# Kernel tuning notes

Hardware: AMD Instinct MI355X
Metric: run time of the kernel (lower is better)

The kernel has to match this reference:

```python
import jax, jax.numpy as jnp
import numpy as np

B, T, D, H = 8, 4096, 1024, 8  # batch, seq_len, width, num_heads


def setup_inputs() -> dict:
    key = jax.random.key(0)
    k0, k1, k2, k3 = jax.random.split(key, 4)
    bw = D // H
    std = (1.0 / bw) ** 0.5  # w_init_variance_scale=1.0
    x = jax.random.normal(k0, (B, T, D), dtype=jnp.float32)
    segment_pos = jnp.tile(jnp.arange(T, dtype=jnp.int32)[None, :], (B, 1))
    ig_w = (jax.random.normal(k1, (H, bw, bw), dtype=jnp.float32) * std)
    ig_b = jnp.zeros((H, bw), dtype=jnp.float32)
    ag_w = (jax.random.normal(k2, (H, bw, bw), dtype=jnp.float32) * std)
    ag_b = jnp.zeros((H, bw), dtype=jnp.float32)
    # rnn_param_init: a_param = log(u^{-0.5} - 1), u ~ U(min_rad^2+eps, max_rad^2+eps)
    eps = 1e-8
    u = jax.random.uniform(k3, (D,), minval=0.9 ** 2 + eps, maxval=0.999 ** 2 + eps)
    a_param = jnp.log(jnp.exp(-0.5 * jnp.log(u)) - 1.0).astype(jnp.float32)
    return dict(x=x, segment_pos=segment_pos, a_param=a_param,
                ig_w=ig_w, ig_b=ig_b, ag_w=ag_w, ag_b=ag_b)


def _block_linear(x, w, b):
    # x: [B,T,D] -> blocks [B,T,H,bw]; y = x_blocks @ w[h] + b[h]
    Bx, Tx, Dx = x.shape
    h, bw = w.shape[0], w.shape[1]
    xb = x.reshape(Bx, Tx, h, bw)
    y = jnp.einsum('bthi,hij->bthj', xb, w) + b
    return y.reshape(Bx, Tx, Dx)


def _rglru(x, a_param, ig_w, ig_b, ag_w, ag_b, sqrt_fn):
    gate_x = jax.nn.sigmoid(_block_linear(x, ig_w, ig_b))
    gate_a = jax.nn.sigmoid(_block_linear(x, ag_w, ag_b))
    log_a = -8.0 * gate_a * jax.nn.softplus(a_param)  # [B,T,D]
    a = jnp.exp(log_a)
    a2 = jnp.exp(2.0 * log_a)
    multiplier = sqrt_fn(jnp.maximum(1.0 - a2, 1e-7))
    normed_x = x * gate_x * multiplier
    # closed-form scan: h_t = p_{t} * sum_{s<=t} normed_x_s / p_s, p = prefix cumprod of a
    p = jnp.cumprod(a, axis=1)
    p_prefix = jnp.concatenate([jnp.ones_like(p[:, :1]), p[:, :-1]], axis=1)
    p_prefix = jnp.maximum(p_prefix, 1e-7)
    S = jnp.cumsum(normed_x / p_prefix, axis=1)
    h = p_prefix * S  # h0 = 0 so alpha term vanishes
    return h, h[:, -1, :]


def reference(x, segment_pos, a_param, ig_w, ig_b, ag_w, ag_b):
    y, last_h = _rglru(x, a_param, ig_w, ig_b, ag_w, ag_b, jnp.sqrt)
    return y, last_h
```

## Files before the change

kernel.cpp:

```cpp
#include <hip/hip_runtime.h>
#include <math.h>

namespace {
constexpr int B = 8, T = 4096, D = 1024, H = 8, BW = 128;
constexpr int C = 128;
constexpr int L = T / C;
constexpr size_t BCD = (size_t)B * C * D;
constexpr size_t BTD = (size_t)B * T * D;
constexpr int WFRAG_N = H * 2 * 2 * 4 * 8 * 64 * 8;

typedef __attribute__((ext_vector_type(8))) short short8v;
typedef __attribute__((ext_vector_type(4))) float float4v;

__device__ __forceinline__ float fast_rcp(float x) { return __builtin_amdgcn_rcpf(x); }
__device__ __forceinline__ float fast_sigmoid(float z) {
    return fast_rcp(1.f + __expf(-z));
}
__device__ __forceinline__ unsigned short bf16_trunc(float x) {
    return (unsigned short)(__float_as_uint(x) >> 16);
}
__device__ __forceinline__ float bf16_tof(unsigned short u) {
    return __uint_as_float((unsigned)u << 16);
}
}

__global__ void k0_wsplit(const float* __restrict__ ig_w,
                          const float* __restrict__ ag_w,
                          unsigned short* __restrict__ wfrag)
{
    const int idx  = blockIdx.x * 256 + threadIdx.x;
    const int e    = idx & 7;
    const int lane = (idx >> 3) & 63;
    const int nt   = (idx >> 9) & 7;
    const int kt   = (idx >> 12) & 3;
    const int s    = (idx >> 14) & 1;
    const int g    = (idx >> 15) & 1;
    const int h    = (idx >> 16) & 7;
    const int k = kt * 32 + (lane >> 4) * 8 + e;
    const int n = nt * 16 + (lane & 15);
    const float w = (g ? ag_w : ig_w)[(size_t)h * BW * BW + (size_t)k * BW + n];
    const unsigned short hi = bf16_trunc(w);
    wfrag[idx] = s ? bf16_trunc(w - bf16_tof(hi)) : hi;
}

__global__ __launch_bounds__(256) void k1_gates(
    const float* __restrict__ x, const float* __restrict__ a_param,
    const float* __restrict__ ig_b, const float* __restrict__ ag_b,
    const unsigned short* __restrict__ wfrag,
    float* __restrict__ log_a, float* __restrict__ nx_out,
    float* __restrict__ logSum)
{
    __shared__ unsigned short xsh[L * BW];
    __shared__ unsigned short xsl[L * BW];

    const int bid = blockIdx.x;
    const int h   = bid & 7;
    const int c   = (bid >> 3) & (C - 1);
    const int b   = bid >> 10;
    const int tid  = threadIdx.x;
    const int wid  = tid >> 6;
    const int lane = tid & 63;
    const int t0   = c * L;

    for (int u = tid; u < L * 32; u += 256) {
        const int row = u >> 5;
        const int c4  = (u & 31) * 4;
        const float4 v = *(const float4*)&x[((size_t)(b * T + t0 + row)) * D + h * BW + c4];
        const float vv[4] = {v.x, v.y, v.z, v.w};
        short4 hv, lv;
        {
            unsigned short h0 = bf16_trunc(vv[0]), h1 = bf16_trunc(vv[1]);
            unsigned short h2 = bf16_trunc(vv[2]), h3 = bf16_trunc(vv[3]);
            hv.x = (short)h0; hv.y = (short)h1; hv.z = (short)h2; hv.w = (short)h3;
            lv.x = (short)bf16_trunc(vv[0] - bf16_tof(h0));
            lv.y = (short)bf16_trunc(vv[1] - bf16_tof(h1));
            lv.z = (short)bf16_trunc(vv[2] - bf16_tof(h2));
            lv.w = (short)bf16_trunc(vv[3] - bf16_tof(h3));
        }
        unsigned byte = (unsigned)(row * 256 + c4 * 2);
        byte ^= (unsigned)((row & 7) << 4);
        *(short4*)((char*)xsh + byte) = hv;
        *(short4*)((char*)xsl + byte) = lv;
    }
    __syncthreads();

    const float4v zero4 = {0.f, 0.f, 0.f, 0.f};
    float4v acc[2][2][2];
    #pragma unroll
    for (int g = 0; g < 2; ++g)
        #pragma unroll
        for (int mt = 0; mt < 2; ++mt)
            #pragma unroll
            for (int ntl = 0; ntl < 2; ++ntl) acc[g][mt][ntl] = zero4;

    #pragma unroll
    for (int kt = 0; kt < 4; ++kt) {
        short8v a[2][2];
        #pragma unroll
        for (int mt = 0; mt < 2; ++mt) {
            const int r = mt * 16 + (lane & 15);
            unsigned byte = (unsigned)(r * 256 + kt * 64 + (lane >> 4) * 16);
            byte ^= (unsigned)((r & 7) << 4);
            a[mt][0] = *(const short8v*)((const char*)xsh + byte);
            a[mt][1] = *(const short8v*)((const char*)xsl + byte);
        }
        short8v bb[2][2][2];
        #pragma unroll
        for (int g = 0; g < 2; ++g)
            #pragma unroll
            for (int ntl = 0; ntl < 2; ++ntl)
                #pragma unroll
                for (int s = 0; s < 2; ++s) {
                    const int ntg = wid * 2 + ntl;
                    const size_t fi =
                        ((((((size_t)h * 2 + g) * 2 + s) * 4 + kt) * 8 + ntg) * 64 + lane) * 8;
                    bb[g][ntl][s] = *(const short8v*)&wfrag[fi];
                }
        #pragma unroll
        for (int g = 0; g < 2; ++g)
            #pragma unroll
            for (int mt = 0; mt < 2; ++mt)
                #pragma unroll
                for (int ntl = 0; ntl < 2; ++ntl) {
                    acc[g][mt][ntl] = __builtin_amdgcn_mfma_f32_16x16x32_bf16(
                        a[mt][0], bb[g][ntl][0], acc[g][mt][ntl], 0, 0, 0);
                    acc[g][mt][ntl] = __builtin_amdgcn_mfma_f32_16x16x32_bf16(
                        a[mt][0], bb[g][ntl][1], acc[g][mt][ntl], 0, 0, 0);
                    acc[g][mt][ntl] = __builtin_amdgcn_mfma_f32_16x16x32_bf16(
                        a[mt][1], bb[g][ntl][0], acc[g][mt][ntl], 0, 0, 0);
                }
    }

    float sp2[2], bi2[2], ba2[2], csum[2] = {0.f, 0.f};
    #pragma unroll
    for (int ntl = 0; ntl < 2; ++ntl) {
        const int col = wid * 32 + ntl * 16 + (lane & 15);
        sp2[ntl] = log1pf(__expf(a_param[h * BW + col]));
        bi2[ntl] = ig_b[h * BW + col];
        ba2[ntl] = ag_b[h * BW + col];
    }
    #pragma unroll
    for (int mt = 0; mt < 2; ++mt)
        #pragma unroll
        for (int ntl = 0; ntl < 2; ++ntl) {
            const int col = wid * 32 + ntl * 16 + (lane & 15);
            #pragma unroll
            for (int e = 0; e < 4; ++e) {
                const int tl = mt * 16 + ((lane >> 4) & 3) * 4 + e;
                const float gx = fast_sigmoid(acc[0][mt][ntl][e] + bi2[ntl]);
                const float ga = fast_sigmoid(acc[1][mt][ntl][e] + ba2[ntl]);
                const float la = -8.f * ga * sp2[ntl];
                const float a2 = __expf(2.f * la);
                const float mu = sqrtf(fmaxf(1.f - a2, 1e-7f));
                unsigned byte = (unsigned)(tl * 256 + col * 2);
                byte ^= (unsigned)((tl & 7) << 4);
                const float xv =
                    bf16_tof(*(const unsigned short*)((const char*)xsh + byte)) +
                    bf16_tof(*(const unsigned short*)((const char*)xsl + byte));
                const size_t gi = ((size_t)(b * T + t0 + tl)) * D + h * BW + col;
                log_a[gi]  = la;
                nx_out[gi] = xv * gx * mu;
                csum[ntl] += la;
            }
        }
    #pragma unroll
    for (int ntl = 0; ntl < 2; ++ntl) {
        float v = csum[ntl];
        v += __shfl_xor(v, 16);
        v += __shfl_xor(v, 32);
        if ((lane & 48) == 0) {
            const int col = wid * 32 + ntl * 16 + lane;
            logSum[((size_t)(b * C + c)) * D + h * BW + col] = v;
        }
    }
}

__global__ void k_scan(float* __restrict__ s)
{
    const int g = blockIdx.x * blockDim.x + threadIdx.x;
    const int b = g >> 10, d = g & 1023;
    const size_t base = (size_t)b * C * D + d;
    float off = 0.f;
    for (int c0 = 0; c0 < C; c0 += 8) {
        float v[8];
        #pragma unroll
        for (int j = 0; j < 8; ++j) v[j] = s[base + (size_t)(c0 + j) * D];
        #pragma unroll
        for (int j = 0; j < 8; ++j) {
            s[base + (size_t)(c0 + j) * D] = off;
            off += v[j];
        }
    }
}

__global__ __launch_bounds__(256) void k3_zsum(
    const float* __restrict__ log_a, const float* __restrict__ nx,
    const float* __restrict__ logOff, float* __restrict__ Zsum)
{
    const int c = blockIdx.x & (C - 1), b = blockIdx.x >> 7;
    const int d = threadIdx.x * 4;
    const size_t cb = ((size_t)(b * C + c)) * D + d;
    float lp[4], zs[4] = {0.f, 0.f, 0.f, 0.f};
    *(float4*)lp = *(const float4*)&logOff[cb];
    size_t base = ((size_t)(b * T + c * L)) * D + d;
    float la4[4], nv4[4], lan[4], nvn[4];
    *(float4*)lan = *(const float4*)&log_a[base];
    *(float4*)nvn = *(const float4*)&nx[base];
    #pragma unroll 4
    for (int t = 0; t < L; ++t) {
        *(float4*)la4 = *(const float4*)lan;
        *(float4*)nv4 = *(const float4*)nvn;
        if (t + 1 < L) {
            *(float4*)lan = *(const float4*)&log_a[base + D];
            *(float4*)nvn = *(const float4*)&nx[base + D];
        }
        #pragma unroll
        for (int k = 0; k < 4; ++k) {
            const float qq = fmaxf(__expf(lp[k]), 1e-7f);
            zs[k] += nv4[k] * fast_rcp(qq);
            lp[k] += la4[k];
        }
        base += D;
    }
    *(float4*)&Zsum[cb] = *(const float4*)zs;
}

__global__ __launch_bounds__(256) void k5_final(
    const float* __restrict__ log_a, const float* __restrict__ logOff,
    const float* __restrict__ Zoff, float* y ,
    float* __restrict__ last_h)
{
    const int c = blockIdx.x & (C - 1), b = blockIdx.x >> 7;
    const int d = threadIdx.x * 4;
    const size_t cb = ((size_t)(b * C + c)) * D + d;
    float lp[4], S[4], h4[4] = {0.f, 0.f, 0.f, 0.f};
    *(float4*)lp = *(const float4*)&logOff[cb];
    *(float4*)S  = *(const float4*)&Zoff[cb];
    size_t base = ((size_t)(b * T + c * L)) * D + d;
    float la4[4], nv4[4], lan[4], nvn[4];
    *(float4*)lan = *(const float4*)&log_a[base];
    *(float4*)nvn = *(const float4*)&y[base];
    #pragma unroll 4
    for (int t = 0; t < L; ++t) {
        *(float4*)la4 = *(const float4*)lan;
        *(float4*)nv4 = *(const float4*)nvn;
        if (t + 1 < L) {
            *(float4*)lan = *(const float4*)&log_a[base + D];
            *(float4*)nvn = *(const float4*)&y[base + D];
        }
        #pragma unroll
        for (int k = 0; k < 4; ++k) {
            const float qq = fmaxf(__expf(lp[k]), 1e-7f);
            S[k] += nv4[k] * fast_rcp(qq);
            h4[k] = qq * S[k];
            lp[k] += la4[k];
        }
        *(float4*)&y[base] = *(const float4*)h4;
        base += D;
    }
    if (c == C - 1)
        *(float4*)&last_h[(size_t)b * D + d] = *(const float4*)h4;
}

extern "C" void kernel_launch(void* const* d_in, const int* in_sizes, int n_in,
                              void* d_out, int out_size, void* d_ws, size_t ws_size,
                              hipStream_t stream)
{
    const float* x       = (const float*)d_in[0];
    const float* a_param = (const float*)d_in[2];
    const float* ig_w    = (const float*)d_in[3];
    const float* ig_b    = (const float*)d_in[4];
    const float* ag_w    = (const float*)d_in[5];
    const float* ag_b    = (const float*)d_in[6];

    float* out    = (float*)d_out;
    float* y      = out;
    float* last_h = out + BTD;

    float* w    = (float*)d_ws;
    float* logS = w;
    float* Zs   = w + BCD;
    float* la   = w + 2 * BCD;
    unsigned short* wfrag = (unsigned short*)Zs;

    k0_wsplit<<<WFRAG_N / 256, 256, 0, stream>>>(ig_w, ag_w, wfrag);
    k1_gates <<<B * C * H, 256, 0, stream>>>(x, a_param, ig_b, ag_b, wfrag,
                                             la, y, logS);
    k_scan   <<<(B * D) / 256, 256, 0, stream>>>(logS);
    k3_zsum  <<<B * C, 256, 0, stream>>>(la, y, logS, Zs);
    k_scan   <<<(B * D) / 256, 256, 0, stream>>>(Zs);
    k5_final <<<B * C, 256, 0, stream>>>(la, logS, Zs, y, last_h);
}
```

Baseline: 431.8 us.

## Transpose chunk summaries, use wave-shuffle scan, and enlarge gate tiles with B prefetch

Stores the per-chunk log-sum and Z-sum arrays in a [B,D,C] layout. The chunk scan becomes a single-wave shuffle-based prefix over contiguous memory instead of a serial strided loop per column. The gate kernel now processes 64-row tiles with 512 threads (two halves of 32 rows) and prefetches the next k-step's weight fragments into registers. The scan kernels also use deeper unrolling. The cost is strided scalar loads and stores of the chunk summaries in k3/k5, plus higher register pressure in k1.

```diff
diff --git a/kernel.cpp b/kernel.cpp
--- a/kernel.cpp
+++ b/kernel.cpp
@@ -5,6 +5,7 @@
 constexpr int B = 8, T = 4096, D = 1024, H = 8, BW = 128;
 constexpr int C = 128;
 constexpr int L = T / C;
+constexpr int KROWS = 64;
 constexpr size_t BCD = (size_t)B * C * D;
 constexpr size_t BTD = (size_t)B * T * D;
 constexpr int WFRAG_N = H * 2 * 2 * 4 * 8 * 64 * 8;
@@ -43,26 +44,29 @@
     wfrag[idx] = s ? bf16_trunc(w - bf16_tof(hi)) : hi;
 }
 
-__global__ __launch_bounds__(256) void k1_gates(
+__global__ __launch_bounds__(512) void k1_gates(
     const float* __restrict__ x, const float* __restrict__ a_param,
     const float* __restrict__ ig_b, const float* __restrict__ ag_b,
     const unsigned short* __restrict__ wfrag,
     float* __restrict__ log_a, float* __restrict__ nx_out,
     float* __restrict__ logSum)
 {
-    __shared__ unsigned short xsh[L * BW];
-    __shared__ unsigned short xsl[L * BW];
-
-    const int bid = blockIdx.x;
-    const int h   = bid & 7;
-    const int c   = (bid >> 3) & (C - 1);
-    const int b   = bid >> 10;
-    const int tid  = threadIdx.x;
-    const int wid  = tid >> 6;
-    const int lane = tid & 63;
-    const int t0   = c * L;
-
-    for (int u = tid; u < L * 32; u += 256) {
+    __shared__ unsigned short xsh[KROWS * BW];
+    __shared__ unsigned short xsl[KROWS * BW];
+
+    const int bid  = blockIdx.x;
+    const int h    = bid & 7;
+    const int tile = (bid >> 3) & 63;
+    const int b    = bid >> 9;
+    const int tid   = threadIdx.x;
+    const int wid   = tid >> 6;
+    const int lane  = tid & 63;
+    const int half  = wid >> 2;
+    const int nquad = wid & 3;
+    const int t0    = tile * KROWS;
+    const int rbase = half * 32;
+
+    for (int u = tid; u < KROWS * 32; u += 512) {
         const int row = u >> 5;
         const int c4  = (u & 31) * 4;
         const float4 v = *(const float4*)&x[((size_t)(b * T + t0 + row)) * D + h * BW + c4];
@@ -93,29 +97,31 @@
             #pragma unroll
             for (int ntl = 0; ntl < 2; ++ntl) acc[g][mt][ntl] = zero4;
 
+#define LOADB(dst, ktv)                                                          \
+    _Pragma("unroll") for (int g = 0; g < 2; ++g)                                \
+    _Pragma("unroll") for (int ntl = 0; ntl < 2; ++ntl)                          \
+    _Pragma("unroll") for (int s = 0; s < 2; ++s) {                              \
+        const int ntg = nquad * 2 + ntl;                                         \
+        const size_t fi =                                                        \
+            ((((((size_t)h * 2 + g) * 2 + s) * 4 + (ktv)) * 8 + ntg) * 64 + lane) * 8; \
+        dst[g][ntl][s] = *(const short8v*)&wfrag[fi];                            \
+    }
+
+    short8v bb[2][2][2];
+    LOADB(bb, 0)
     #pragma unroll
     for (int kt = 0; kt < 4; ++kt) {
+        short8v bbn[2][2][2];
+        if (kt < 3) { LOADB(bbn, kt + 1) }
         short8v a[2][2];
         #pragma unroll
         for (int mt = 0; mt < 2; ++mt) {
-            const int r = mt * 16 + (lane & 15);
+            const int r = rbase + mt * 16 + (lane & 15);
             unsigned byte = (unsigned)(r * 256 + kt * 64 + (lane >> 4) * 16);
             byte ^= (unsigned)((r & 7) << 4);
             a[mt][0] = *(const short8v*)((const char*)xsh + byte);
             a[mt][1] = *(const short8v*)((const char*)xsl + byte);
         }
-        short8v bb[2][2][2];
-        #pragma unroll
-        for (int g = 0; g < 2; ++g)
-            #pragma unroll
-            for (int ntl = 0; ntl < 2; ++ntl)
-                #pragma unroll
-                for (int s = 0; s < 2; ++s) {
-                    const int ntg = wid * 2 + ntl;
-                    const size_t fi =
-                        ((((((size_t)h * 2 + g) * 2 + s) * 4 + kt) * 8 + ntg) * 64 + lane) * 8;
-                    bb[g][ntl][s] = *(const short8v*)&wfrag[fi];
-                }
         #pragma unroll
         for (int g = 0; g < 2; ++g)
             #pragma unroll
@@ -129,12 +135,21 @@
                     acc[g][mt][ntl] = __builtin_amdgcn_mfma_f32_16x16x32_bf16(
                         a[mt][1], bb[g][ntl][0], acc[g][mt][ntl], 0, 0, 0);
                 }
-    }
+        if (kt < 3) {
+            #pragma unroll
+            for (int g = 0; g < 2; ++g)
+                #pragma unroll
+                for (int ntl = 0; ntl < 2; ++ntl)
+                    #pragma unroll
+                    for (int s = 0; s < 2; ++s) bb[g][ntl][s] = bbn[g][ntl][s];
+        }
+    }
+#undef LOADB
 
     float sp2[2], bi2[2], ba2[2], csum[2] = {0.f, 0.f};
     #pragma unroll
     for (int ntl = 0; ntl < 2; ++ntl) {
-        const int col = wid * 32 + ntl * 16 + (lane & 15);
+        const int col = nquad * 32 + ntl * 16 + (lane & 15);
         sp2[ntl] = log1pf(__expf(a_param[h * BW + col]));
         bi2[ntl] = ig_b[h * BW + col];
         ba2[ntl] = ag_b[h * BW + col];
@@ -143,10 +158,10 @@
     for (int mt = 0; mt < 2; ++mt)
         #pragma unroll
         for (int ntl = 0; ntl < 2; ++ntl) {
-            const int col = wid * 32 + ntl * 16 + (lane & 15);
+            const int col = nquad * 32 + ntl * 16 + (lane & 15);
             #pragma unroll
             for (int e = 0; e < 4; ++e) {
-                const int tl = mt * 16 + ((lane >> 4) & 3) * 4 + e;
+                const int tl = rbase + mt * 16 + ((lane >> 4) & 3) * 4 + e;
                 const float gx = fast_sigmoid(acc[0][mt][ntl][e] + bi2[ntl]);
                 const float ga = fast_sigmoid(acc[1][mt][ntl][e] + ba2[ntl]);
                 const float la = -8.f * ga * sp2[ntl];
@@ -163,34 +178,37 @@
                 csum[ntl] += la;
             }
         }
+    const int cc = tile * 2 + half;
     #pragma unroll
     for (int ntl = 0; ntl < 2; ++ntl) {
         float v = csum[ntl];
         v += __shfl_xor(v, 16);
         v += __shfl_xor(v, 32);
         if ((lane & 48) == 0) {
-            const int col = wid * 32 + ntl * 16 + lane;
-            logSum[((size_t)(b * C + c)) * D + h * BW + col] = v;
-        }
-    }
-}
-
-__global__ void k_scan(float* __restrict__ s)
-{
-    const int g = blockIdx.x * blockDim.x + threadIdx.x;
-    const int b = g >> 10, d = g & 1023;
-    const size_t base = (size_t)b * C * D + d;
-    float off = 0.f;
-    for (int c0 = 0; c0 < C; c0 += 8) {
-        float v[8];
-        #pragma unroll
-        for (int j = 0; j < 8; ++j) v[j] = s[base + (size_t)(c0 + j) * D];
-        #pragma unroll
-        for (int j = 0; j < 8; ++j) {
-            s[base + (size_t)(c0 + j) * D] = off;
-            off += v[j];
-        }
-    }
+            const int col = nquad * 32 + ntl * 16 + lane;
+            logSum[((size_t)b * D + h * BW + col) * C + cc] = v;
+        }
+    }
+}
+
+__global__ __launch_bounds__(256) void k_scan(float* __restrict__ s)
+{
+    const int wid  = threadIdx.x >> 6;
+    const int lane = threadIdx.x & 63;
+    const int g    = blockIdx.x * 4 + wid;
+    const size_t base = (size_t)g * C;
+    const float s0 = s[base + 2 * lane];
+    const float s1 = s[base + 2 * lane + 1];
+    const float pair = s0 + s1;
+    float p = pair;
+    #pragma unroll
+    for (int off = 1; off < 64; off <<= 1) {
+        const float v = __shfl_up(p, off);
+        if (lane >= off) p += v;
+    }
+    const float excl = p - pair;
+    s[base + 2 * lane]     = excl;
+    s[base + 2 * lane + 1] = excl + s0;
 }
 
 __global__ __launch_bounds__(256) void k3_zsum(
@@ -199,15 +217,17 @@
 {
     const int c = blockIdx.x & (C - 1), b = blockIdx.x >> 7;
     const int d = threadIdx.x * 4;
-    const size_t cb = ((size_t)(b * C + c)) * D + d;
     float lp[4], zs[4] = {0.f, 0.f, 0.f, 0.f};
-    *(float4*)lp = *(const float4*)&logOff[cb];
+    #pragma unroll
+    for (int k = 0; k < 4; ++k)
+        lp[k] = logOff[((size_t)b * D + d + k) * C + c];
     size_t base = ((size_t)(b * T + c * L)) * D + d;
-    float la4[4], nv4[4], lan[4], nvn[4];
+    float lan[4], nvn[4];
     *(float4*)lan = *(const float4*)&log_a[base];
     *(float4*)nvn = *(const float4*)&nx[base];
-    #pragma unroll 4
+    #pragma unroll 8
     for (int t = 0; t < L; ++t) {
+        float la4[4], nv4[4];
         *(float4*)la4 = *(const float4*)lan;
         *(float4*)nv4 = *(const float4*)nvn;
         if (t + 1 < L) {
@@ -222,7 +242,9 @@
         }
         base += D;
     }
-    *(float4*)&Zsum[cb] = *(const float4*)zs;
+    #pragma unroll
+    for (int k = 0; k < 4; ++k)
+        Zsum[((size_t)b * D + d + k) * C + c] = zs[k];
 }
 
 __global__ __launch_bounds__(256) void k5_final(
@@ -232,16 +254,19 @@
 {
     const int c = blockIdx.x & (C - 1), b = blockIdx.x >> 7;
     const int d = threadIdx.x * 4;
-    const size_t cb = ((size_t)(b * C + c)) * D + d;
     float lp[4], S[4], h4[4] = {0.f, 0.f, 0.f, 0.f};
-    *(float4*)lp = *(const float4*)&logOff[cb];
-    *(float4*)S  = *(const float4*)&Zoff[cb];
+    #pragma unroll
+    for (int k = 0; k < 4; ++k) {
+        lp[k] = logOff[((size_t)b * D + d + k) * C + c];
+        S[k]  = Zoff[((size_t)b * D + d + k) * C + c];
+    }
     size_t base = ((size_t)(b * T + c * L)) * D + d;
-    float la4[4], nv4[4], lan[4], nvn[4];
+    float lan[4], nvn[4];
     *(float4*)lan = *(const float4*)&log_a[base];
     *(float4*)nvn = *(const float4*)&y[base];
-    #pragma unroll 4
+    #pragma unroll 8
     for (int t = 0; t < L; ++t) {
+        float la4[4], nv4[4];
         *(float4*)la4 = *(const float4*)lan;
         *(float4*)nv4 = *(const float4*)nvn;
         if (t + 1 < L) {
@@ -284,10 +309,10 @@
     unsigned short* wfrag = (unsigned short*)Zs;
 
     k0_wsplit<<<WFRAG_N / 256, 256, 0, stream>>>(ig_w, ag_w, wfrag);
-    k1_gates <<<B * C * H, 256, 0, stream>>>(x, a_param, ig_b, ag_b, wfrag,
-                                             la, y, logS);
-    k_scan   <<<(B * D) / 256, 256, 0, stream>>>(logS);
+    k1_gates <<<B * (T / KROWS) * H, 512, 0, stream>>>(x, a_param, ig_b, ag_b,
+                                                       wfrag, la, y, logS);
+    k_scan   <<<(B * D) / 4, 256, 0, stream>>>(logS);
     k3_zsum  <<<B * C, 256, 0, stream>>>(la, y, logS, Zs);
-    k_scan   <<<(B * D) / 256, 256, 0, stream>>>(Zs);
+    k_scan   <<<(B * D) / 4, 256, 0, stream>>>(Zs);
     k5_final <<<B * C, 256, 0, stream>>>(la, logS, Zs, y, last_h);
 }
```

Result: slower. 459.5 us (+6.4%).
